# Kernel optimization log

Measured on AMD Instinct MI355X. Metric: run time of the kernel, lower is better.

## Reference

```python
import jax, jax.numpy as jnp
import numpy as np

D_BLADE = 256
D_FFN = 1024
N_TOK = 8192
LN_EPS = 1e-5


def _derive_cayley_table():
    basis_gens = [(), (1,), (2,), (3,), (1, 2), (1, 3), (2, 3), (1, 2, 3)]
    gens_to_idx = {g: i for i, g in enumerate(basis_gens)}

    def reduce(a, b):
        gens = list(a) + list(b)
        sign = 1
        changed = True
        while changed:
            changed = False
            i = 0
            while i < len(gens) - 1:
                if gens[i] == gens[i + 1]:
                    gens.pop(i); gens.pop(i)
                    changed = True
                    if i > 0:
                        i -= 1
                elif gens[i] > gens[i + 1]:
                    gens[i], gens[i + 1] = gens[i + 1], gens[i]
                    sign *= -1
                    changed = True
                    i += 1
                else:
                    i += 1
        return gens_to_idx[tuple(gens)], sign

    return [[reduce(basis_gens[i], basis_gens[j]) for j in range(8)] for i in range(8)]


def _sparse_cayley():
    table = _derive_cayley_table()
    si, sj, tk, sg = [], [], [], []
    for i in range(8):
        for j in range(8):
            k, s = table[i][j]
            si.append(i); sj.append(j); tk.append(k); sg.append(float(s))
    return (np.array(si, np.int64), np.array(sj, np.int64),
            np.array(tk, np.int64), np.array(sg, np.float32))


def setup_inputs() -> dict:
    key = jax.random.key(0)
    ks = jax.random.split(key, 6)
    si, sj, tk, sg = _sparse_cayley()
    inv_d = 1.0 / np.sqrt(D_BLADE)
    inv_f = 1.0 / np.sqrt(D_FFN)
    return {
        "x": jax.random.normal(ks[0], (N_TOK, 8, D_BLADE), jnp.float32),
        "iw": jnp.full((64,), 0.1, jnp.float32),
        "sg": jnp.asarray(sg),
        "gg": jnp.asarray(0.5, jnp.float32),
        "gate_w": jax.random.normal(ks[1], (D_FFN, D_BLADE), jnp.float32) * inv_d,
        "up_w": jax.random.normal(ks[2], (D_FFN, D_BLADE), jnp.float32) * inv_d,
        "down_w": jax.random.normal(ks[3], (D_BLADE, D_FFN), jnp.float32) * inv_f,
        "ln_w": jnp.ones((D_BLADE,), jnp.float32),
        "ln_b": jnp.zeros((D_BLADE,), jnp.float32),
        "si": jnp.asarray(si),
        "sj": jnp.asarray(sj),
        "tk": jnp.asarray(tk),
    }


def reference(x, iw, sg, gg, gate_w, up_w, down_w, ln_w, ln_b, si, sj, tk):
    # x: (N, 8, D). 64 Cayley pairs: gather blades i,j, multiply, scatter-add to k.
    w = jax.nn.sigmoid(iw)                                  # (64,)
    products = x[:, si, :] * x[:, sj, :] * (sg * w)[None, :, None]  # (N,64,D)
    geo = jnp.zeros_like(x).at[:, tk, :].add(products)      # (N,8,D)
    g = jax.nn.sigmoid(gg)
    mixed = g * geo + (1.0 - g) * x
    # LayerNorm over last dim
    mu = jnp.mean(mixed, axis=-1, keepdims=True)
    var = jnp.mean(jnp.square(mixed - mu), axis=-1, keepdims=True)
    normed = (mixed - mu) * jax.lax.rsqrt(var + LN_EPS) * ln_w + ln_b
    # SwiGLU FFN
    h = jax.nn.silu(jnp.einsum("nbd,fd->nbf", normed, gate_w)) \
        * jnp.einsum("nbd,fd->nbf", normed, up_w)
    out = jnp.einsum("nbf,df->nbd", h, down_w)
    return x + out
```

## Files before the change

kernel.cpp:

```cpp
#include <hip/hip_runtime.h>
#include <hip/hip_bf16.h>

#define D_BLADE 256
#define D_FFN 1024
#define N_TOK 8192
#define M_TOTAL (N_TOK * 8)

typedef __attribute__((ext_vector_type(8))) short bf16x8;
typedef __attribute__((ext_vector_type(4))) float f32x4;
typedef __attribute__((address_space(1))) void gvoid;
typedef __attribute__((address_space(3))) void svoid;

__device__ __forceinline__ float sigm(float v) { return 1.0f / (1.0f + __expf(-v)); }

__global__ __launch_bounds__(256) void wconv_kernel(const float* __restrict__ g,
                                                    const float* __restrict__ u,
                                                    const float* __restrict__ dn,
                                                    __hip_bfloat16* __restrict__ wgu,
                                                    __hip_bfloat16* __restrict__ dwb) {
    int i = blockIdx.x * 256 + threadIdx.x;
    int f = i >> 8, k = i & 255;
    int t = f >> 4, fi = f & 15;
    wgu[(size_t)(t * 32 + fi) * 256 + k]      = __float2bfloat16(g[i]);
    wgu[(size_t)(t * 32 + 16 + fi) * 256 + k] = __float2bfloat16(u[i]);
    dwb[i] = __float2bfloat16(dn[i]);
}

__global__ __launch_bounds__(256) void geo_ln_kernel(
    const float* __restrict__ x, const float* __restrict__ iw,
    const float* __restrict__ sg, const float* __restrict__ gg,
    const float* __restrict__ lnw, const float* __restrict__ lnb,
    __hip_bfloat16* __restrict__ nrm)
{
    static constexpr int CK[64] = {
        0,1,2,3,4,5,6,7,
        1,0,4,5,2,3,7,6,
        2,4,0,6,1,7,3,5,
        3,5,6,0,7,1,2,4,
        4,2,1,7,0,6,5,3,
        5,3,7,1,6,0,4,2,
        6,7,3,2,5,4,0,1,
        7,6,5,4,3,2,1,0};
    __shared__ float coefs[64];
    __shared__ float redA[4][8];
    __shared__ float redB[4][8];
    const int tid = threadIdx.x;
    const int n = blockIdx.x;
    if (tid < 64) coefs[tid] = sg[tid] * sigm(iw[tid]);
    __syncthreads();

    const float* xp = x + (size_t)n * (8 * D_BLADE) + tid;
    float xa[8];
#pragma unroll
    for (int b = 0; b < 8; ++b) xa[b] = xp[b * D_BLADE];

    float geo[8] = {0.f,0.f,0.f,0.f,0.f,0.f,0.f,0.f};
#pragma unroll
    for (int p = 0; p < 64; ++p)
        geo[CK[p]] += coefs[p] * xa[p >> 3] * xa[p & 7];

    const float g = sigm(gg[0]);
    float mixed[8], sm[8], sq[8];
#pragma unroll
    for (int b = 0; b < 8; ++b) {
        mixed[b] = g * geo[b] + (1.0f - g) * xa[b];
        sm[b] = mixed[b];
        sq[b] = mixed[b] * mixed[b];
    }
#pragma unroll
    for (int off = 32; off > 0; off >>= 1) {
#pragma unroll
        for (int b = 0; b < 8; ++b) {
            sm[b] += __shfl_xor(sm[b], off, 64);
            sq[b] += __shfl_xor(sq[b], off, 64);
        }
    }
    const int wv = tid >> 6;
    if ((tid & 63) == 0) {
#pragma unroll
        for (int b = 0; b < 8; ++b) { redA[wv][b] = sm[b]; redB[wv][b] = sq[b]; }
    }
    __syncthreads();

    const float lw = lnw[tid], lb = lnb[tid];
    __hip_bfloat16* op = nrm + ((size_t)n * 8) * D_BLADE + tid;
#pragma unroll
    for (int b = 0; b < 8; ++b) {
        float ts = redA[0][b] + redA[1][b] + redA[2][b] + redA[3][b];
        float tq = redB[0][b] + redB[1][b] + redB[2][b] + redB[3][b];
        float mu = ts * (1.0f / 256.0f);
        float var = tq * (1.0f / 256.0f) - mu * mu;
        float rs = rsqrtf(var + 1e-5f);
        op[b * D_BLADE] = __float2bfloat16((mixed[b] - mu) * rs * lw + lb);
    }
}


#define STAGE(dst, srcbase, rowstride, kofs, NLOADS)                                 \
    _Pragma("unroll")                                                                 \
    for (int i = 0; i < (NLOADS); ++i) {                                              \
        int L = i * 4096 + tid * 16;                                                  \
        int r = L >> 7;                                                               \
        int Xs = (L & 127) ^ ((r & 7) << 4);                                          \
        const __hip_bfloat16* sp = (srcbase) + (size_t)(r) * (rowstride) + (kofs) + (Xs >> 1); \
        __builtin_amdgcn_global_load_lds((gvoid*)sp, (svoid*)((dst) + L), 16, 0, 0);  \
    }

__global__ __launch_bounds__(256, 4) void gu_kernel(
    const __hip_bfloat16* __restrict__ nrm,
    const __hip_bfloat16* __restrict__ wgu,
    __hip_bfloat16* __restrict__ h,
    int mbase)
{
    __shared__ char lds[32768];
    char* sA = lds;
    char* sB = lds + 16384;

    const int tid = threadIdx.x;
    const int l = tid & 63;
    const int w = tid >> 6;
    const int wm = w >> 1, wn = w & 1;
    const int rr = l & 15;
    const int kq = l >> 4;
    const int bm = blockIdx.x >> 4;
    const int n0 = (blockIdx.x & 15) * 128;
    const int m0 = mbase + bm * 128;
    const int hr0 = bm * 128;
    const __hip_bfloat16* An = nrm + (size_t)m0 * D_BLADE;
    const __hip_bfloat16* Bn = wgu + (size_t)n0 * D_BLADE;

    const f32x4 zero = {0.f, 0.f, 0.f, 0.f};
    f32x4 acc[4][4];
#pragma unroll
    for (int mt = 0; mt < 4; ++mt)
#pragma unroll
        for (int nt = 0; nt < 4; ++nt) acc[mt][nt] = zero;

    const int rsw = (rr & 7) << 4;

    STAGE(sA, An, D_BLADE, 0, 4)
    STAGE(sB, Bn, D_BLADE, 0, 4)
    asm volatile("s_waitcnt vmcnt(0)" ::: "memory");
    __syncthreads();

    for (int c = 0; c < 4; ++c) {
#pragma unroll
        for (int kk = 0; kk < 2; ++kk) {
            const int cb = (kk * 64 + kq * 16) ^ rsw;
            bf16x8 a[4], b[4];
#pragma unroll
            for (int nt = 0; nt < 4; ++nt)
                b[nt] = *reinterpret_cast<const bf16x8*>(sB + (wn * 64 + nt * 16 + rr) * 128 + cb);
#pragma unroll
            for (int mt = 0; mt < 4; ++mt)
                a[mt] = *reinterpret_cast<const bf16x8*>(sA + (wm * 64 + mt * 16 + rr) * 128 + cb);
            __builtin_amdgcn_s_setprio(1);
#pragma unroll
            for (int mt = 0; mt < 4; ++mt)
#pragma unroll
                for (int nt = 0; nt < 4; ++nt)
                    acc[mt][nt] = __builtin_amdgcn_mfma_f32_16x16x32_bf16(a[mt], b[nt], acc[mt][nt], 0, 0, 0);
            __builtin_amdgcn_s_setprio(0);
        }
        __syncthreads();
        if (c < 3) {
            STAGE(sA, An, D_BLADE, (c + 1) * 64, 4)
            STAGE(sB, Bn, D_BLADE, (c + 1) * 64, 4)
            asm volatile("s_waitcnt vmcnt(0)" ::: "memory");
            __syncthreads();
        }
    }

#pragma unroll
    for (int mt = 0; mt < 4; ++mt)
#pragma unroll
        for (int ntp = 0; ntp < 2; ++ntp) {
            f32x4 gv = acc[mt][2 * ntp];
            f32x4 uv = acc[mt][2 * ntp + 1];
            const int fcol = ((n0 + wn * 64) >> 1) + ntp * 16 + rr;
#pragma unroll
            for (int r = 0; r < 4; ++r) {
                int row = hr0 + wm * 64 + mt * 16 + kq * 4 + r;
                float ge = gv[r];
                float hv = ge * sigm(ge) * uv[r];
                h[(size_t)row * D_FFN + fcol] = __float2bfloat16(hv);
            }
        }
}

__global__ __launch_bounds__(256, 2) void down_kernel(
    const __hip_bfloat16* __restrict__ h,
    const __hip_bfloat16* __restrict__ dwb,
    const float* __restrict__ x,
    float* __restrict__ out,
    int mbase)
{
    __shared__ char lds[49152];
    char* sA = lds;
    char* sB = lds + 16384;

    const int tid = threadIdx.x;
    const int l = tid & 63;
    const int w = tid >> 6;
    const int wm = w >> 1, wn = w & 1;
    const int rr = l & 15;
    const int kq = l >> 4;
    const int rsw = (rr & 7) << 4;
    const int bm = blockIdx.x;
    const int hr0 = bm * 128;
    const __hip_bfloat16* An = h + (size_t)hr0 * D_FFN;
    const __hip_bfloat16* Bn = dwb;

    const f32x4 zero = {0.f, 0.f, 0.f, 0.f};
    f32x4 acc[4][8];
#pragma unroll
    for (int mt = 0; mt < 4; ++mt)
#pragma unroll
        for (int nt = 0; nt < 8; ++nt) acc[mt][nt] = zero;

    STAGE(sA, An, D_FFN, 0, 4)
    STAGE(sB, Bn, D_FFN, 0, 8)
    asm volatile("s_waitcnt vmcnt(0)" ::: "memory");
    __builtin_amdgcn_sched_barrier(0);
    __syncthreads();

    for (int c = 0; c < 16; ++c) {
#pragma unroll
        for (int kk = 0; kk < 2; ++kk) {
            const int cb = (kk * 64 + kq * 16) ^ rsw;
            bf16x8 a[4], b[8];
#pragma unroll
            for (int nt = 0; nt < 8; ++nt)
                b[nt] = *reinterpret_cast<const bf16x8*>(sB + (wn * 128 + nt * 16 + rr) * 128 + cb);
#pragma unroll
            for (int mt = 0; mt < 4; ++mt)
                a[mt] = *reinterpret_cast<const bf16x8*>(sA + (wm * 64 + mt * 16 + rr) * 128 + cb);
            __builtin_amdgcn_s_setprio(1);
#pragma unroll
            for (int mt = 0; mt < 4; ++mt)
#pragma unroll
                for (int nt = 0; nt < 8; ++nt)
                    acc[mt][nt] = __builtin_amdgcn_mfma_f32_16x16x32_bf16(a[mt], b[nt], acc[mt][nt], 0, 0, 0);
            __builtin_amdgcn_s_setprio(0);
        }
        __syncthreads();
        if (c < 15) {
            STAGE(sA, An, D_FFN, (c + 1) * 64, 4)
            STAGE(sB, Bn, D_FFN, (c + 1) * 64, 8)
            asm volatile("s_waitcnt vmcnt(0)" ::: "memory");
            __builtin_amdgcn_sched_barrier(0);
            __syncthreads();
        }
    }

#pragma unroll
    for (int mt = 0; mt < 4; ++mt)
#pragma unroll
        for (int nt = 0; nt < 8; ++nt)
#pragma unroll
            for (int r = 0; r < 4; ++r) {
                int gm = mbase + hr0 + wm * 64 + mt * 16 + kq * 4 + r;
                int d = wn * 128 + nt * 16 + rr;
                size_t idx = (size_t)gm * D_BLADE + d;
                out[idx] = x[idx] + acc[mt][nt][r];
            }
}

extern "C" void kernel_launch(void* const* d_in, const int* in_sizes, int n_in,
                              void* d_out, int out_size, void* d_ws, size_t ws_size,
                              hipStream_t stream) {
    const float* x   = (const float*)d_in[0];
    const float* iw  = (const float*)d_in[1];
    const float* sg  = (const float*)d_in[2];
    const float* gg  = (const float*)d_in[3];
    const float* gwf = (const float*)d_in[4];
    const float* uwf = (const float*)d_in[5];
    const float* dwf = (const float*)d_in[6];
    const float* lnw = (const float*)d_in[7];
    const float* lnb = (const float*)d_in[8];
    float* out = (float*)d_out;

    char* ws = (char*)d_ws;
    __hip_bfloat16* nrm = (__hip_bfloat16*)ws;
    size_t off = (size_t)M_TOTAL * D_BLADE * 2;
    __hip_bfloat16* wgu = (__hip_bfloat16*)(ws + off);
    off += (size_t)2 * D_FFN * D_BLADE * 2;
    __hip_bfloat16* dwb = (__hip_bfloat16*)(ws + off);
    off += (size_t)D_FFN * D_BLADE * 2;
    __hip_bfloat16* h = (__hip_bfloat16*)(ws + off);

    int S = 1;
    while (S < 64 && off + ((size_t)M_TOTAL / S) * D_FFN * 2 > ws_size) S <<= 1;
    const int MS = M_TOTAL / S;

    wconv_kernel<<<dim3((D_FFN * D_BLADE) / 256), dim3(256), 0, stream>>>(gwf, uwf, dwf, wgu, dwb);
    geo_ln_kernel<<<dim3(N_TOK), dim3(256), 0, stream>>>(x, iw, sg, gg, lnw, lnb, nrm);
    for (int s = 0; s < S; ++s) {
        gu_kernel<<<dim3((MS / 128) * 16), dim3(256), 0, stream>>>(nrm, wgu, h, s * MS);
        down_kernel<<<dim3(MS / 128), dim3(256), 0, stream>>>(h, dwb, x, out, s * MS);
    }
}
```

Baseline: 200.3 us.

## Double-buffer LDS staging with 32-wide K chunks in both GEMM kernels

```diff
diff --git a/kernel.cpp b/kernel.cpp
--- a/kernel.cpp
+++ b/kernel.cpp
@@ -96,12 +96,13 @@
 }
 
 
-#define STAGE(dst, srcbase, rowstride, kofs, NLOADS)                                 \
+#define STAGE32(dst, srcbase, rowstride, kofs, NLOADS)                               \
     _Pragma("unroll")                                                                 \
     for (int i = 0; i < (NLOADS); ++i) {                                              \
         int L = i * 4096 + tid * 16;                                                  \
-        int r = L >> 7;                                                               \
-        int Xs = (L & 127) ^ ((r & 7) << 4);                                          \
+        int r = L >> 6;                                                               \
+        int X = L & 63;                                                               \
+        int Xs = X ^ ((r & 3) << 4);                                                  \
         const __hip_bfloat16* sp = (srcbase) + (size_t)(r) * (rowstride) + (kofs) + (Xs >> 1); \
         __builtin_amdgcn_global_load_lds((gvoid*)sp, (svoid*)((dst) + L), 16, 0, 0);  \
     }
@@ -113,8 +114,6 @@
     int mbase)
 {
     __shared__ char lds[32768];
-    char* sA = lds;
-    char* sB = lds + 16384;
 
     const int tid = threadIdx.x;
     const int l = tid & 63;
@@ -122,6 +121,8 @@
     const int wm = w >> 1, wn = w & 1;
     const int rr = l & 15;
     const int kq = l >> 4;
+    const int cb = (kq * 16) ^ ((rr & 3) << 4);
+
     const int bm = blockIdx.x >> 4;
     const int n0 = (blockIdx.x & 15) * 128;
     const int m0 = mbase + bm * 128;
@@ -136,37 +137,42 @@
 #pragma unroll
         for (int nt = 0; nt < 4; ++nt) acc[mt][nt] = zero;
 
-    const int rsw = (rr & 7) << 4;
-
-    STAGE(sA, An, D_BLADE, 0, 4)
-    STAGE(sB, Bn, D_BLADE, 0, 4)
+    {
+        char* sA = lds;
+        char* sB = lds + 8192;
+        STAGE32(sA, An, D_BLADE, 0, 2)
+        STAGE32(sB, Bn, D_BLADE, 0, 2)
+    }
     asm volatile("s_waitcnt vmcnt(0)" ::: "memory");
+    __builtin_amdgcn_sched_barrier(0);
     __syncthreads();
 
-    for (int c = 0; c < 4; ++c) {
-#pragma unroll
-        for (int kk = 0; kk < 2; ++kk) {
-            const int cb = (kk * 64 + kq * 16) ^ rsw;
-            bf16x8 a[4], b[4];
+    for (int c = 0; c < 8; ++c) {
+        char* cbuf = lds + (c & 1) * 16384;
+        if (c < 7) {
+            char* nbuf = lds + ((c + 1) & 1) * 16384;
+            STAGE32(nbuf, An, D_BLADE, (c + 1) * 32, 2)
+            STAGE32(nbuf + 8192, Bn, D_BLADE, (c + 1) * 32, 2)
+        }
+        const char* sA = cbuf;
+        const char* sB = cbuf + 8192;
+        bf16x8 a[4], b[4];
+#pragma unroll
+        for (int nt = 0; nt < 4; ++nt)
+            b[nt] = *reinterpret_cast<const bf16x8*>(sB + (wn * 64 + nt * 16 + rr) * 64 + cb);
+#pragma unroll
+        for (int mt = 0; mt < 4; ++mt)
+            a[mt] = *reinterpret_cast<const bf16x8*>(sA + (wm * 64 + mt * 16 + rr) * 64 + cb);
+        __builtin_amdgcn_s_setprio(1);
+#pragma unroll
+        for (int mt = 0; mt < 4; ++mt)
 #pragma unroll
             for (int nt = 0; nt < 4; ++nt)
-                b[nt] = *reinterpret_cast<const bf16x8*>(sB + (wn * 64 + nt * 16 + rr) * 128 + cb);
-#pragma unroll
-            for (int mt = 0; mt < 4; ++mt)
-                a[mt] = *reinterpret_cast<const bf16x8*>(sA + (wm * 64 + mt * 16 + rr) * 128 + cb);
-            __builtin_amdgcn_s_setprio(1);
-#pragma unroll
-            for (int mt = 0; mt < 4; ++mt)
-#pragma unroll
-                for (int nt = 0; nt < 4; ++nt)
-                    acc[mt][nt] = __builtin_amdgcn_mfma_f32_16x16x32_bf16(a[mt], b[nt], acc[mt][nt], 0, 0, 0);
-            __builtin_amdgcn_s_setprio(0);
-        }
-        __syncthreads();
-        if (c < 3) {
-            STAGE(sA, An, D_BLADE, (c + 1) * 64, 4)
-            STAGE(sB, Bn, D_BLADE, (c + 1) * 64, 4)
+                acc[mt][nt] = __builtin_amdgcn_mfma_f32_16x16x32_bf16(a[mt], b[nt], acc[mt][nt], 0, 0, 0);
+        __builtin_amdgcn_s_setprio(0);
+        if (c < 7) {
             asm volatile("s_waitcnt vmcnt(0)" ::: "memory");
+            __builtin_amdgcn_sched_barrier(0);
             __syncthreads();
         }
     }
@@ -196,8 +202,6 @@
     int mbase)
 {
     __shared__ char lds[49152];
-    char* sA = lds;
-    char* sB = lds + 16384;
 
     const int tid = threadIdx.x;
     const int l = tid & 63;
@@ -205,7 +209,8 @@
     const int wm = w >> 1, wn = w & 1;
     const int rr = l & 15;
     const int kq = l >> 4;
-    const int rsw = (rr & 7) << 4;
+    const int cb = (kq * 16) ^ ((rr & 3) << 4);
+
     const int bm = blockIdx.x;
     const int hr0 = bm * 128;
     const __hip_bfloat16* An = h + (size_t)hr0 * D_FFN;
@@ -218,35 +223,40 @@
 #pragma unroll
         for (int nt = 0; nt < 8; ++nt) acc[mt][nt] = zero;
 
-    STAGE(sA, An, D_FFN, 0, 4)
-    STAGE(sB, Bn, D_FFN, 0, 8)
+    {
+        char* sA = lds;
+        char* sB = lds + 8192;
+        STAGE32(sA, An, D_FFN, 0, 2)
+        STAGE32(sB, Bn, D_FFN, 0, 4)
+    }
     asm volatile("s_waitcnt vmcnt(0)" ::: "memory");
     __builtin_amdgcn_sched_barrier(0);
     __syncthreads();
 
-    for (int c = 0; c < 16; ++c) {
-#pragma unroll
-        for (int kk = 0; kk < 2; ++kk) {
-            const int cb = (kk * 64 + kq * 16) ^ rsw;
-            bf16x8 a[4], b[8];
+    for (int c = 0; c < 32; ++c) {
+        char* cbuf = lds + (c & 1) * 24576;
+        if (c < 31) {
+            char* nbuf = lds + ((c + 1) & 1) * 24576;
+            STAGE32(nbuf, An, D_FFN, (c + 1) * 32, 2)
+            STAGE32(nbuf + 8192, Bn, D_FFN, (c + 1) * 32, 4)
+        }
+        const char* sA = cbuf;
+        const char* sB = cbuf + 8192;
+        bf16x8 a[4], b[8];
+#pragma unroll
+        for (int nt = 0; nt < 8; ++nt)
+            b[nt] = *reinterpret_cast<const bf16x8*>(sB + (wn * 128 + nt * 16 + rr) * 64 + cb);
+#pragma unroll
+        for (int mt = 0; mt < 4; ++mt)
+            a[mt] = *reinterpret_cast<const bf16x8*>(sA + (wm * 64 + mt * 16 + rr) * 64 + cb);
+        __builtin_amdgcn_s_setprio(1);
+#pragma unroll
+        for (int mt = 0; mt < 4; ++mt)
 #pragma unroll
             for (int nt = 0; nt < 8; ++nt)
-                b[nt] = *reinterpret_cast<const bf16x8*>(sB + (wn * 128 + nt * 16 + rr) * 128 + cb);
-#pragma unroll
-            for (int mt = 0; mt < 4; ++mt)
-                a[mt] = *reinterpret_cast<const bf16x8*>(sA + (wm * 64 + mt * 16 + rr) * 128 + cb);
-            __builtin_amdgcn_s_setprio(1);
-#pragma unroll
-            for (int mt = 0; mt < 4; ++mt)
-#pragma unroll
-                for (int nt = 0; nt < 8; ++nt)
-                    acc[mt][nt] = __builtin_amdgcn_mfma_f32_16x16x32_bf16(a[mt], b[nt], acc[mt][nt], 0, 0, 0);
-            __builtin_amdgcn_s_setprio(0);
-        }
-        __syncthreads();
-        if (c < 15) {
-            STAGE(sA, An, D_FFN, (c + 1) * 64, 4)
-            STAGE(sB, Bn, D_FFN, (c + 1) * 64, 8)
+                acc[mt][nt] = __builtin_amdgcn_mfma_f32_16x16x32_bf16(a[mt], b[nt], acc[mt][nt], 0, 0, 0);
+        __builtin_amdgcn_s_setprio(0);
+        if (c < 31) {
             asm volatile("s_waitcnt vmcnt(0)" ::: "memory");
             __builtin_amdgcn_sched_barrier(0);
             __syncthreads();
```

After: 209.6 us. 1.05x slower.
